# Optimization experiments

Measured on AMD Instinct MI355X. Metric: run time of the kernel, lower is better.

Reference implementation:

```python
import jax, jax.numpy as jnp
import numpy as np

B, S, C = 4, 2048, 1024
DK = C // 4   # 256, q/k projection dim
DO = 1024     # out_channels


def setup_inputs() -> dict:
    key = jax.random.key(0)
    ks = jax.random.split(key, 7)
    s = 1.0 / np.sqrt(C)
    return {
        "x": jax.random.normal(ks[0], (B, S, C), dtype=jnp.float32),
        "Wq": jax.random.uniform(ks[1], (C, DK), jnp.float32, -s, s),
        "bq": jax.random.uniform(ks[2], (DK,), jnp.float32, -s, s),
        "Wk": jax.random.uniform(ks[3], (C, DK), jnp.float32, -s, s),
        "bk": jax.random.uniform(ks[4], (DK,), jnp.float32, -s, s),
        "Wv": jax.random.uniform(ks[5], (C, DO), jnp.float32, -s, s),
        "bv": jax.random.uniform(ks[6], (DO,), jnp.float32, -s, s),
    }


def reference(x, Wq, bq, Wk, bk, Wv, bv):
    q = jnp.einsum("bsc,cd->bsd", x, Wq) + bq   # [B,S,DK]
    k = jnp.einsum("bsc,cd->bsd", x, Wk) + bk   # [B,S,DK]
    v = jnp.einsum("bsc,cd->bsd", x, Wv) + bv   # [B,S,DO]
    scores = jnp.einsum("bqd,bkd->bqk", q, k) / jnp.sqrt(jnp.float32(DK))
    attn = jax.nn.softmax(scores, axis=-1)      # [B,S,S]
    return jnp.einsum("bqk,bkd->bqd", attn, v)  # [B,S,DO]
```

## Files before the change

### kernel.cpp

```cpp
#include <hip/hip_runtime.h>
#include <hip/hip_bf16.h>

typedef __attribute__((ext_vector_type(8))) short short8;
typedef __attribute__((ext_vector_type(8))) __bf16 bf16x8;
typedef __attribute__((ext_vector_type(4))) float f32x4;

#define MFMA(a, b, c) __builtin_amdgcn_mfma_f32_16x16x32_bf16((a), (b), (c), 0, 0, 0)
#define SCALE 0.0625f

static __device__ __forceinline__ void gload16(const void* g, void* l) {
  __builtin_amdgcn_global_load_lds(
      (const __attribute__((address_space(1))) void*)g,
      (__attribute__((address_space(3))) void*)l, 16, 0, 0);
}

static __device__ __forceinline__ unsigned short f2b(float f) {
  union { __hip_bfloat16 h; unsigned short u; } cv;
  cv.h = __float2bfloat16(f);
  return cv.u;
}

__global__ __launch_bounds__(256) void prep_kern(
    const float* __restrict__ x, unsigned short* __restrict__ xb,
    const float* __restrict__ bq, const float* __restrict__ bk,
    const float* __restrict__ bv, float* __restrict__ bc,
    const float* __restrict__ Wq, const float* __restrict__ Wk,
    const float* __restrict__ Wv, unsigned short* __restrict__ wt) {
  __shared__ __align__(16) unsigned short tile[64][72];
  int bid = blockIdx.x, t = threadIdx.x;
  if (bid < 4096) {
    long i = ((long)bid * 256 + t) * 8;
    float4 a = *reinterpret_cast<const float4*>(x + i);
    float4 b = *reinterpret_cast<const float4*>(x + i + 4);
    short8 o;
    o[0] = (short)f2b(a.x); o[1] = (short)f2b(a.y); o[2] = (short)f2b(a.z); o[3] = (short)f2b(a.w);
    o[4] = (short)f2b(b.x); o[5] = (short)f2b(b.y); o[6] = (short)f2b(b.z); o[7] = (short)f2b(b.w);
    *reinterpret_cast<short8*>(xb + i) = o;
    return;
  }
  if (bid < 4102) {
    int i = (bid - 4096) * 256 + t;
    float v = (i < 256) ? bq[i] : (i < 512) ? bk[i - 256] : bv[i - 512];
    bc[i] = v;
    return;
  }
  const float* src; unsigned short* dst; int ldsrc, lam;
  if (bid < 4166)      { lam = bid - 4102; src = Wq; dst = wt;              ldsrc = 256;
                         lam = (lam & 3) | ((lam >> 2) << 8); }
  else if (bid < 4230) { lam = bid - 4166; src = Wk; dst = wt + 256 * 1024; ldsrc = 256;
                         lam = (lam & 3) | ((lam >> 2) << 8); }
  else                 { lam = bid - 4230; src = Wv; dst = wt + 512 * 1024; ldsrc = 1024;
                         lam = (lam & 15) | ((lam >> 4) << 8); }
  int c0 = (lam & 255) * 64, r0 = (lam >> 8) * 64;
  #pragma unroll
  for (int it = 0; it < 4; ++it) {
    int idx = it * 1024 + t * 4;
    int row = idx >> 6, col = idx & 63;
    float4 v = *reinterpret_cast<const float4*>(src + (long)(r0 + row) * ldsrc + c0 + col);
    tile[row][col + 0] = f2b(v.x); tile[row][col + 1] = f2b(v.y);
    tile[row][col + 2] = f2b(v.z); tile[row][col + 3] = f2b(v.w);
  }
  __syncthreads();
  #pragma unroll
  for (int it = 0; it < 4; ++it) {
    int idx = it * 1024 + t * 4;
    int orow = idx >> 6, ocol = idx & 63;
    ushort4 o;
    o.x = tile[ocol + 0][orow]; o.y = tile[ocol + 1][orow];
    o.z = tile[ocol + 2][orow]; o.w = tile[ocol + 3][orow];
    *reinterpret_cast<ushort4*>(dst + (long)(c0 + orow) * 1024 + r0 + ocol) = o;
  }
}

template <int SWZ, int BN, bool BIAS, bool VSPLIT, bool EXPSUM>
__global__ __launch_bounds__(512, 2) void gemm_pi(
    const unsigned short* __restrict__ A, const unsigned short* __restrict__ B,
    const float* __restrict__ bias, void* __restrict__ Cout,
    int NT, int lda, int ldb, int ldc,
    long batchA, long batchB, long batchC,
    float* __restrict__ lpart,
    unsigned short* __restrict__ vT) {
  constexpr int WM = 128;
  constexpr int WN = BN / 4;
  constexpr int NF = BN / 64;
  constexpr int BR = BN / 64;
  constexpr int ASH = 256 * 64;
  constexpr int TSH = ASH + BN * 64;
  __shared__ __align__(128) unsigned short lds[2 * TSH];

  int bid = blockIdx.x;
  int b = 0, tm, tn;
  if constexpr (SWZ == 0) {
    int xcd = bid & 7, s = bid >> 3;
    tm = xcd * 4 + (s >> 3); tn = s & 7;
  } else {
    int xcd = bid & 7, s = bid >> 3;
    b = xcd >> 1; tm = (xcd & 1) * 4 + (s >> 3); tn = s & 7;
  }

  int t = threadIdx.x, w = t >> 6, l = t & 63;
  int wr = w >> 2, wc = w & 3;
  int g = l >> 4, c = l & 15;

  f32x4 acc[8][NF];
  #pragma unroll
  for (int m = 0; m < 8; ++m)
    #pragma unroll
    for (int n = 0; n < NF; ++n) acc[m][n] = (f32x4){0.f, 0.f, 0.f, 0.f};

  int srow = t >> 3;
  int scb = (t & 7) * 16;
  const unsigned short* aptr = A + (long)b * batchA + (long)(tm * 256) * lda;
  const unsigned short* bptr = B + (long)b * batchB + (long)(tn * BN) * ldb;
  int kb = scb ^ ((srow & 7) << 4);

  auto stageA = [&](int buf, int k0, int r) {
    int row = r * 64 + srow;
    gload16(aptr + (long)row * lda + k0 + (kb >> 1),
            lds + buf * TSH + r * 4096 + t * 8);
  };
  auto stageB = [&](int buf, int k0, int r) {
    int row = r * 64 + srow;
    gload16(bptr + (long)row * ldb + k0 + (kb >> 1),
            lds + buf * TSH + ASH + r * 4096 + t * 8);
  };
  auto ldA = [&](const char* abase, int mh, int kh, int m) {
    int row = wr * WM + mh * 64 + m * 16 + c;
    int pb = row * 128 + (kh * 32 + g * 8) * 2;
    pb ^= ((pb >> 7) & 7) << 4;
    return *reinterpret_cast<const bf16x8*>(abase + pb);
  };
  auto ldB = [&](const char* bbase, int kh, int n) {
    int row = wc * WN + n * 16 + c;
    int pb = row * 128 + (kh * 32 + g * 8) * 2;
    pb ^= ((pb >> 7) & 7) << 4;
    return *reinterpret_cast<const bf16x8*>(bbase + pb);
  };

  #pragma unroll
  for (int r = 0; r < BR; ++r) stageB(0, 0, r);
  stageA(0, 0, 0); stageA(0, 0, 2); stageA(0, 0, 1); stageA(0, 0, 3);
  asm volatile("s_waitcnt vmcnt(0)" ::: "memory");
  __builtin_amdgcn_s_barrier();

  for (int kt = 0; kt < NT; ++kt) {
    int cur = kt & 1, nb = cur ^ 1;
    const char* abase = (const char*)(lds + cur * TSH);
    const char* bbase = (const char*)(lds + cur * TSH + ASH);
    bool more = (kt + 1) < NT;
    int k1 = (kt + 1) * 64;
    bf16x8 bfr[NF];
    #pragma unroll
    for (int p = 0; p < 4; ++p) {
      const int kh = p >> 1, mh = p & 1;
      bf16x8 af[4];
      #pragma unroll
      for (int m = 0; m < 4; ++m) af[m] = ldA(abase, mh, kh, m);
      if (mh == 0) {
        #pragma unroll
        for (int n = 0; n < NF; ++n) bfr[n] = ldB(bbase, kh, n);
      }
      if (more) {
        if constexpr (BN == 256) {
          if      (p == 0) { stageB(nb, k1, 0); stageB(nb, k1, 1); }
          else if (p == 1) { stageB(nb, k1, 2); stageB(nb, k1, 3); }
          else if (p == 2) { stageA(nb, k1, 0); stageA(nb, k1, 2); }
          else             { stageA(nb, k1, 1); stageA(nb, k1, 3); }
        } else {
          if      (p == 0) { stageB(nb, k1, 0); stageB(nb, k1, 1); stageB(nb, k1, 2); }
          else if (p == 1) { stageA(nb, k1, 0); stageA(nb, k1, 2); }
          else if (p == 2) { stageA(nb, k1, 1); stageA(nb, k1, 3); }
        }
      }
      __builtin_amdgcn_s_barrier();
      asm volatile("s_waitcnt lgkmcnt(0)" ::: "memory");
      __builtin_amdgcn_sched_barrier(0);
      __builtin_amdgcn_s_setprio(1);
      #pragma unroll
      for (int m = 0; m < 4; ++m)
        #pragma unroll
        for (int n = 0; n < NF; ++n)
          acc[mh * 4 + m][n] = MFMA(af[m], bfr[n], acc[mh * 4 + m][n]);
      __builtin_amdgcn_s_setprio(0);
      if (p == 0) {
        if (kt == NT - 1) asm volatile("s_waitcnt vmcnt(0)" ::: "memory");
        else if (BN == 256) asm volatile("s_waitcnt vmcnt(2)" ::: "memory");
        else                asm volatile("s_waitcnt vmcnt(3)" ::: "memory");
      }
      if (p == 3 && more) {
        asm volatile("s_waitcnt vmcnt(2)" ::: "memory");
      }
      __builtin_amdgcn_s_barrier();
    }
  }

  int rbase = tm * 256 + wr * WM + g * 4;
  int c0 = tn * BN + wc * WN + c;

  if constexpr (EXPSUM) {
    __shared__ float lred[4][256];
    #pragma unroll
    for (int mi = 0; mi < 8; ++mi) {
      int roff = (mi / 4) * 64 + (mi % 4) * 16;
      #pragma unroll
      for (int j = 0; j < 4; ++j) {
        long ob = (long)b * batchC + (long)(rbase + roff + j) * ldc + c0;
        float rs = 0.f;
        #pragma unroll
        for (int n = 0; n < NF; ++n) {
          float pv = __expf(acc[mi][n][j] * SCALE);
          ((unsigned short*)Cout)[ob + n * 16] = f2b(pv);
          rs += pv;
        }
        rs += __shfl_xor(rs, 1); rs += __shfl_xor(rs, 2);
        rs += __shfl_xor(rs, 4); rs += __shfl_xor(rs, 8);
        if (c == 0) lred[wc][wr * WM + roff + g * 4 + j] = rs;
      }
    }
    __syncthreads();
    for (int rr = t; rr < 256; rr += 512) {
      float s = lred[0][rr] + lred[1][rr] + lred[2][rr] + lred[3][rr];
      lpart[((long)b * 2048 + tm * 256 + rr) * 8 + tn] = s;
    }
  } else {
    #pragma unroll
    for (int mi = 0; mi < 8; ++mi) {
      int roff = (mi / 4) * 64 + (mi % 4) * 16;
      int s0 = (rbase + roff) & 2047;
      #pragma unroll
      for (int n = 0; n < NF; ++n) {
        int col = c0 + n * 16;
        float bv = BIAS ? bias[col] : 0.f;
        if (VSPLIT && (col - c) >= 512) {
          int bb = tm >> 3;
          ushort4 pk;
          pk.x = f2b(acc[mi][n][0] + bv); pk.y = f2b(acc[mi][n][1] + bv);
          pk.z = f2b(acc[mi][n][2] + bv); pk.w = f2b(acc[mi][n][3] + bv);
          *reinterpret_cast<ushort4*>(vT + (long)bb * 2097152 +
                                      (long)(col - 512) * 2048 + s0) = pk;
        } else {
          long rowb = (long)b * batchC + (long)(rbase + roff) * ldc + col;
          #pragma unroll
          for (int j = 0; j < 4; ++j)
            ((unsigned short*)Cout)[rowb + (long)j * ldc] = f2b(acc[mi][n][j] + bv);
        }
      }
    }
  }
}

__global__ __launch_bounds__(1024, 4) void gemm_pv(
    const unsigned short* __restrict__ A,
    const unsigned short* __restrict__ B,
    float* __restrict__ Cout,
    const float* __restrict__ lpart) {
  constexpr int NT = 32;
  constexpr int ASH = 128 * 64;
  constexpr int TSH = ASH + 256 * 64;
  __shared__ __align__(128) unsigned short lds[3 * TSH];
  __shared__ float linv_s[128];

  int bid = blockIdx.x;
  int xcd = bid & 7, sidx = bid >> 3;
  int b = xcd >> 1;
  int tm = (xcd & 1) * 8 + (sidx >> 2), tn = sidx & 3;

  int t = threadIdx.x, w = t >> 6, l = t & 63;
  int wr = w >> 2, wc = w & 3;
  int g = l >> 4, c = l & 15;

  if (t < 128) {
    const float* lp = lpart + ((long)b * 2048 + tm * 128 + t) * 8;
    float s = lp[0] + lp[1] + lp[2] + lp[3] + lp[4] + lp[5] + lp[6] + lp[7];
    linv_s[t] = 1.f / s;
  }

  f32x4 acc[2][4];
  #pragma unroll
  for (int m = 0; m < 2; ++m)
    #pragma unroll
    for (int n = 0; n < 4; ++n) acc[m][n] = (f32x4){0.f, 0.f, 0.f, 0.f};

  int srow = t >> 3;
  int scb = (t & 7) * 16;
  int kb = scb ^ ((srow & 7) << 4);
  const unsigned short* aptr = A + (long)b * 4194304 + (long)(tm * 128) * 2048;
  const unsigned short* bptr = B + (long)b * 2097152 + (long)(tn * 256) * 2048;

  auto stage3 = [&](int buf, int kt2) {
    int k0 = kt2 * 64;
    gload16(aptr + (long)srow * 2048 + k0 + (kb >> 1),
            lds + buf * TSH + t * 8);
    #pragma unroll
    for (int r = 0; r < 2; ++r) {
      int row = r * 128 + srow;
      gload16(bptr + (long)row * 2048 + k0 + (kb >> 1),
              lds + buf * TSH + ASH + r * 8192 + t * 8);
    }
  };

  stage3(0, 0); stage3(1, 1);
  asm volatile("s_waitcnt vmcnt(3)" ::: "memory");
  __builtin_amdgcn_s_barrier();

  for (int kt = 0; kt < NT; ++kt) {
    const char* abase = (const char*)(lds + (kt % 3) * TSH);
    const char* bbase = abase + ASH * 2;

    bf16x8 af[2][2], bf[2][4];
    #pragma unroll
    for (int sk = 0; sk < 2; ++sk) {
      #pragma unroll
      for (int m = 0; m < 2; ++m) {
        int p = (wr * 32 + m * 16 + c) * 128 + (sk * 32 + g * 8) * 2;
        p ^= ((p >> 7) & 7) << 4;
        af[sk][m] = *reinterpret_cast<const bf16x8*>(abase + p);
      }
      #pragma unroll
      for (int n = 0; n < 4; ++n) {
        int p = (wc * 64 + n * 16 + c) * 128 + (sk * 32 + g * 8) * 2;
        p ^= ((p >> 7) & 7) << 4;
        bf[sk][n] = *reinterpret_cast<const bf16x8*>(bbase + p);
      }
    }

    if (kt + 2 < NT) stage3((kt + 2) % 3, kt + 2);

    __builtin_amdgcn_s_setprio(1);
    #pragma unroll
    for (int sk = 0; sk < 2; ++sk)
      #pragma unroll
      for (int m = 0; m < 2; ++m)
        #pragma unroll
        for (int n = 0; n < 4; ++n)
          acc[m][n] = MFMA(af[sk][m], bf[sk][n], acc[m][n]);
    __builtin_amdgcn_s_setprio(0);

    if (kt < NT - 1) {
      if (kt == NT - 2) asm volatile("s_waitcnt vmcnt(0)" ::: "memory");
      else              asm volatile("s_waitcnt vmcnt(3)" ::: "memory");
      __builtin_amdgcn_s_barrier();
    }
  }

  int rloc = wr * 32 + g * 4;
  int c0 = tn * 256 + wc * 64 + c;
  #pragma unroll
  for (int mi = 0; mi < 2; ++mi) {
    float lv[4];
    #pragma unroll
    for (int j = 0; j < 4; ++j)
      lv[j] = linv_s[rloc + mi * 16 + j];
    #pragma unroll
    for (int n = 0; n < 4; ++n) {
      long rowb = (long)b * 2097152 + (long)(tm * 128 + rloc + mi * 16) * 1024
                + c0 + n * 16;
      #pragma unroll
      for (int j = 0; j < 4; ++j)
        Cout[rowb + (long)j * 1024] = acc[mi][n][j] * lv[j];
    }
  }
}

extern "C" void kernel_launch(void* const* d_in, const int* in_sizes, int n_in,
                              void* d_out, int out_size, void* d_ws, size_t ws_size,
                              hipStream_t stream) {
  (void)in_sizes; (void)n_in; (void)out_size; (void)ws_size;
  const float* x  = (const float*)d_in[0];
  const float* Wq = (const float*)d_in[1];
  const float* bq = (const float*)d_in[2];
  const float* Wk = (const float*)d_in[3];
  const float* bk = (const float*)d_in[4];
  const float* Wv = (const float*)d_in[5];
  const float* bv = (const float*)d_in[6];
  float* out = (float*)d_out;
  char* ws = (char*)d_ws;

  unsigned short* xb   = (unsigned short*)(ws + 0);
  float*          lpart= (float*)         (ws + 0);
  unsigned short* wt   = (unsigned short*)(ws + 16777216);
  float*          bc   = (float*)         (ws + 19922944);
  unsigned short* qkv  = (unsigned short*)(ws + 19929088);
  unsigned short* vT   = (unsigned short*)(ws + 45094912);
  unsigned short* attn = (unsigned short*)(ws + 61872128);

  prep_kern<<<4486, 256, 0, stream>>>(x, xb, bq, bk, bv, bc, Wq, Wk, Wv, wt);

  gemm_pi<0, 192, true, true, false><<<dim3(256), 512, 0, stream>>>(
      xb, wt, bc, qkv, 16, 1024, 1024, 1536, 0, 0, 0, nullptr, vT);

  gemm_pi<1, 256, false, false, true><<<dim3(256), 512, 0, stream>>>(
      qkv, qkv + 256, nullptr, attn, 4, 1536, 1536, 2048,
      (long)2048 * 1536, (long)2048 * 1536, (long)2048 * 2048, lpart, nullptr);

  gemm_pv<<<dim3(256), 1024, 0, stream>>>(attn, vT, out, lpart);
}
```

Measured before the change: 99.20 us.

## Retile PV GEMM to 128x128 tiles with 256-thread blocks and double buffering

Replaces the 1024-thread PV GEMM (128x256 tile, triple-buffered LDS) with a 256-thread kernel that computes a 128x128 tile per block, with 4x4 MFMA tiles per wave and two LDS buffers. The grid doubles to 512 blocks and each block is smaller, which should allow more blocks per CU and give better load balance. In exchange, each A tile is loaded twice as often, prefetch runs only one stage ahead, and extra barriers are added inside the k-loop.

```diff
diff --git a/kernel.cpp b/kernel.cpp
--- a/kernel.cpp
+++ b/kernel.cpp
@@ -249,24 +249,25 @@
   }
 }
 
-__global__ __launch_bounds__(1024, 4) void gemm_pv(
+__global__ __launch_bounds__(256, 2) void gemm_pv2(
     const unsigned short* __restrict__ A,
     const unsigned short* __restrict__ B,
     float* __restrict__ Cout,
     const float* __restrict__ lpart) {
   constexpr int NT = 32;
   constexpr int ASH = 128 * 64;
-  constexpr int TSH = ASH + 256 * 64;
-  __shared__ __align__(128) unsigned short lds[3 * TSH];
+  constexpr int TSH = 2 * ASH;
+  __shared__ __align__(128) unsigned short lds[2 * TSH];
   __shared__ float linv_s[128];
 
   int bid = blockIdx.x;
   int xcd = bid & 7, sidx = bid >> 3;
   int b = xcd >> 1;
-  int tm = (xcd & 1) * 8 + (sidx >> 2), tn = sidx & 3;
+  int tm = (xcd & 1) * 8 + (sidx >> 3);
+  int tn = sidx & 7;
 
   int t = threadIdx.x, w = t >> 6, l = t & 63;
-  int wr = w >> 2, wc = w & 3;
+  int wr = w >> 1, wc = w & 1;
   int g = l >> 4, c = l & 15;
 
   if (t < 128) {
@@ -275,9 +276,9 @@
     linv_s[t] = 1.f / s;
   }
 
-  f32x4 acc[2][4];
-  #pragma unroll
-  for (int m = 0; m < 2; ++m)
+  f32x4 acc[4][4];
+  #pragma unroll
+  for (int m = 0; m < 4; ++m)
     #pragma unroll
     for (int n = 0; n < 4; ++n) acc[m][n] = (f32x4){0.f, 0.f, 0.f, 0.f};
 
@@ -285,68 +286,68 @@
   int scb = (t & 7) * 16;
   int kb = scb ^ ((srow & 7) << 4);
   const unsigned short* aptr = A + (long)b * 4194304 + (long)(tm * 128) * 2048;
-  const unsigned short* bptr = B + (long)b * 2097152 + (long)(tn * 256) * 2048;
-
-  auto stage3 = [&](int buf, int kt2) {
+  const unsigned short* bptr = B + (long)b * 2097152 + (long)(tn * 128) * 2048;
+
+  auto stage8 = [&](int buf, int kt2) {
     int k0 = kt2 * 64;
-    gload16(aptr + (long)srow * 2048 + k0 + (kb >> 1),
-            lds + buf * TSH + t * 8);
-    #pragma unroll
-    for (int r = 0; r < 2; ++r) {
-      int row = r * 128 + srow;
+    #pragma unroll
+    for (int r = 0; r < 4; ++r) {
+      int row = r * 32 + srow;
+      gload16(aptr + (long)row * 2048 + k0 + (kb >> 1),
+              lds + buf * TSH + r * 2048 + t * 8);
+    }
+    #pragma unroll
+    for (int r = 0; r < 4; ++r) {
+      int row = r * 32 + srow;
       gload16(bptr + (long)row * 2048 + k0 + (kb >> 1),
-              lds + buf * TSH + ASH + r * 8192 + t * 8);
-    }
-  };
-
-  stage3(0, 0); stage3(1, 1);
-  asm volatile("s_waitcnt vmcnt(3)" ::: "memory");
+              lds + buf * TSH + ASH + r * 2048 + t * 8);
+    }
+  };
+
+  stage8(0, 0);
+  asm volatile("s_waitcnt vmcnt(0)" ::: "memory");
   __builtin_amdgcn_s_barrier();
 
   for (int kt = 0; kt < NT; ++kt) {
-    const char* abase = (const char*)(lds + (kt % 3) * TSH);
+    int cur = kt & 1;
+    const char* abase = (const char*)(lds + cur * TSH);
     const char* bbase = abase + ASH * 2;
-
-    bf16x8 af[2][2], bf[2][4];
     #pragma unroll
     for (int sk = 0; sk < 2; ++sk) {
-      #pragma unroll
-      for (int m = 0; m < 2; ++m) {
-        int p = (wr * 32 + m * 16 + c) * 128 + (sk * 32 + g * 8) * 2;
+      bf16x8 af[4], bf[4];
+      #pragma unroll
+      for (int m = 0; m < 4; ++m) {
+        int p = (wr * 64 + m * 16 + c) * 128 + (sk * 32 + g * 8) * 2;
         p ^= ((p >> 7) & 7) << 4;
-        af[sk][m] = *reinterpret_cast<const bf16x8*>(abase + p);
+        af[m] = *reinterpret_cast<const bf16x8*>(abase + p);
       }
       #pragma unroll
       for (int n = 0; n < 4; ++n) {
         int p = (wc * 64 + n * 16 + c) * 128 + (sk * 32 + g * 8) * 2;
         p ^= ((p >> 7) & 7) << 4;
-        bf[sk][n] = *reinterpret_cast<const bf16x8*>(bbase + p);
-      }
-    }
-
-    if (kt + 2 < NT) stage3((kt + 2) % 3, kt + 2);
-
-    __builtin_amdgcn_s_setprio(1);
-    #pragma unroll
-    for (int sk = 0; sk < 2; ++sk)
-      #pragma unroll
-      for (int m = 0; m < 2; ++m)
+        bf[n] = *reinterpret_cast<const bf16x8*>(bbase + p);
+      }
+      if (sk == 0 && kt + 1 < NT) stage8(cur ^ 1, kt + 1);
+      __builtin_amdgcn_s_barrier();
+      asm volatile("s_waitcnt lgkmcnt(0)" ::: "memory");
+      __builtin_amdgcn_sched_barrier(0);
+      __builtin_amdgcn_s_setprio(1);
+      #pragma unroll
+      for (int m = 0; m < 4; ++m)
         #pragma unroll
         for (int n = 0; n < 4; ++n)
-          acc[m][n] = MFMA(af[sk][m], bf[sk][n], acc[m][n]);
-    __builtin_amdgcn_s_setprio(0);
-
-    if (kt < NT - 1) {
-      if (kt == NT - 2) asm volatile("s_waitcnt vmcnt(0)" ::: "memory");
-      else              asm volatile("s_waitcnt vmcnt(3)" ::: "memory");
+          acc[m][n] = MFMA(af[m], bf[n], acc[m][n]);
+      __builtin_amdgcn_s_setprio(0);
+      if (sk == 1 && kt < NT - 1)
+        asm volatile("s_waitcnt vmcnt(0)" ::: "memory");
       __builtin_amdgcn_s_barrier();
     }
   }
 
-  int rloc = wr * 32 + g * 4;
-  int c0 = tn * 256 + wc * 64 + c;
-  #pragma unroll
-  for (int mi = 0; mi < 2; ++mi) {
+  int rloc = wr * 64 + g * 4;
+  int c0 = tn * 128 + wc * 64 + c;
+  #pragma unroll
+  for (int mi = 0; mi < 4; ++mi) {
     float lv[4];
     #pragma unroll
     for (int j = 0; j < 4; ++j)
@@ -393,5 +394,5 @@
       qkv, qkv + 256, nullptr, attn, 4, 1536, 1536, 2048,
       (long)2048 * 1536, (long)2048 * 1536, (long)2048 * 2048, lpart, nullptr);
 
-  gemm_pv<<<dim3(256), 1024, 0, stream>>>(attn, vT, out, lpart);
-}
+  gemm_pv2<<<dim3(512), 256, 0, stream>>>(attn, vT, out, lpart);
+}
```

New measurement: 99.71 us. About the same (+0.5%).
